# Kernel optimization log

Measured on AMD Instinct MI355X. Metric: run time of the kernel, lower is better.

The kernel has to match this reference:

```python
import jax, jax.numpy as jnp
import numpy as np

B, T, D, H = 16, 81, 128, 8  # batch, ntok, d_model (= d_head), n_head


def setup_inputs() -> dict:
    key = jax.random.key(0)
    ks = jax.random.split(key, 6)
    s = 0.02
    return {
        "x": jax.random.normal(ks[0], (B, T, D), jnp.float32),
        "msk": jnp.ones((1, H, T, T), jnp.float32),
        "wqkv_w": jax.random.normal(ks[1], (H * 2 * D, D), jnp.float32) * s,
        "wqkv_b": jax.random.normal(ks[2], (H * 2 * D,), jnp.float32) * s,
        "wk_w": jax.random.normal(ks[3], (H, D), jnp.float32) * s,
        "fanout_w": jax.random.normal(ks[4], (D, D), jnp.float32) * s,
        "fanout_b": jax.random.normal(ks[5], (D,), jnp.float32) * s,
        "head_enabled": jnp.ones((H,), jnp.float32),
        "n": 0, "layer": 0, "pas": 1,
    }


def quick_gelu(x):
    return x * jax.nn.sigmoid(1.702 * x)


def reference(x, msk, wqkv_w, wqkv_b, wk_w, fanout_w, fanout_b, head_enabled, n, layer, pas):
    b, t, d = x.shape
    h = wk_w.shape[0]
    # qkv projection: per-head q and v of full width d (d_head == d_model)
    y = x @ wqkv_w.T + wqkv_b                      # [b, t, h*2*d]
    y = y.reshape(b, t, h, 2 * d)
    q, v = y[..., :d], y[..., d:]                  # [b, t, h, d] each
    # k: input gated per-head by wk.weight rows
    k = x[:, :, None, :] * wk_w[None, None, :, :]  # [b, t, h, d]
    # v gating by head-enabled flags
    v = v * head_enabled[None, None, :, None]
    # L1 attention scores: a[b,h,t,s] = -sum_d |q[b,t,h,d] - k[b,s,h,d]| / sqrt(d)
    diff = jnp.abs(q[:, :, None, :, :] - k[:, None, :, :, :])  # [b, t, s, h, d]
    a = -diff.sum(-1)                               # [b, t, s, h]
    a = jnp.transpose(a, (0, 3, 1, 2)) / jnp.sqrt(jnp.asarray(d, x.dtype))  # [b,h,t,s]
    a = jax.nn.softmax(a, axis=3) * msk
    bo = jnp.einsum('bhts,bshd->bthd', a, v)        # [b, t, h, d]
    bo = bo.sum(axis=2)                             # sum over heads -> [b, t, d]
    ap = jnp.transpose(a[0] - 1.0 + msk[0], (1, 2, 0))  # [t, s, h]
    z = quick_gelu(bo + 4.0) - 4.0
    z = z @ fanout_w.T + fanout_b
    return (x + z, ap)
```

## Files before the change

### kernel.cpp

```cpp
#include <hip/hip_runtime.h>
#include <math.h>

#define Bq 16
#define Tq 81
#define Dq 128
#define Hq 8
#define BT (Bq*Tq)
#define BTD (Bq*Tq*Dq)
#define PS 84
#define P_SZ   (Bq*Tq*Hq*PS)
#define QV_SZ  (BT*Hq*Dq)
#define P_OFF  0
#define Q_OFF  (P_OFF + P_SZ)
#define V_OFF  (Q_OFF + QV_SZ)

#define LSTR 136

typedef __attribute__((ext_vector_type(8))) short short8;
typedef __attribute__((ext_vector_type(4))) float f32x4;
typedef _Float16 h2 __attribute__((ext_vector_type(2)));

__device__ __forceinline__ int imin(int a, int b) { return a < b ? a : b; }
__device__ __forceinline__ unsigned short f2bf(float f) {
    unsigned u = __float_as_uint(f);
    u += 0x7fffu + ((u >> 16) & 1u);
    return (unsigned short)(u >> 16);
}
__device__ __forceinline__ float bf2f(unsigned short s) {
    return __uint_as_float((unsigned)s << 16);
}
__device__ __forceinline__ unsigned pk2h(float a, float b) {
    h2 v; v[0] = (_Float16)a; v[1] = (_Float16)b;
    return *(unsigned*)&v;
}
__device__ __forceinline__ float l1h(unsigned qv, unsigned xv, unsigned wv, float acc) {
    const h2 q = *(const h2*)&qv, xx = *(const h2*)&xv, ww = *(const h2*)&wv;
    h2 d = q - xx * ww;
    unsigned du = (*(unsigned*)&d) & 0x7fff7fffu;
    const h2 da = *(const h2*)&du;
#if __has_builtin(__builtin_amdgcn_fdot2)
    return __builtin_amdgcn_fdot2(da, (h2){(_Float16)1.f, (_Float16)1.f}, acc, false);
#else
    return acc + (float)da[0] + (float)da[1];
#endif
}

__global__ __launch_bounds__(256) void k_qkv_mfma(
    const float* __restrict__ x, const float* __restrict__ wqkv,
    const float* __restrict__ bias, const float* __restrict__ he,
    float* __restrict__ Qo, unsigned short* __restrict__ Vb)
{
    __shared__ unsigned short xs[64 * LSTR];
    __shared__ unsigned short wsh[64 * LSTR];
    const int tid = threadIdx.x;
    const int w = tid >> 6, lane = tid & 63;
    const int ln = lane & 15, quad = lane >> 4;
    const int r0 = blockIdx.x * 64;
    const int n0 = blockIdx.y * 64;
    const int h  = blockIdx.y >> 2;
    const int isV = (blockIdx.y >> 1) & 1;
    const int c0 = (blockIdx.y & 1) * 64;

    #pragma unroll
    for (int i = 0; i < 8; ++i) {
        const int idx = tid + i * 256;
        const int r = idx >> 5, c4 = idx & 31;
        const int gr = imin(r0 + r, BT - 1);
        const float4 v = *(const float4*)(x + (size_t)gr * Dq + c4 * 4);
        ushort4 o;
        o.x = f2bf(v.x); o.y = f2bf(v.y); o.z = f2bf(v.z); o.w = f2bf(v.w);
        *(ushort4*)(&xs[r * LSTR + c4 * 4]) = o;

        const float4 vw = *(const float4*)(wqkv + (size_t)(n0 + r) * Dq + c4 * 4);
        ushort4 ow;
        ow.x = f2bf(vw.x); ow.y = f2bf(vw.y); ow.z = f2bf(vw.z); ow.w = f2bf(vw.w);
        *(ushort4*)(&wsh[r * LSTR + c4 * 4]) = ow;
    }
    __syncthreads();

    const unsigned short* xa = xs + (w * 16 + ln) * LSTR + quad * 8;
    const unsigned short* wb = wsh + ln * LSTR + quad * 8;

    f32x4 acc[4];
    #pragma unroll
    for (int i = 0; i < 4; ++i) acc[i] = (f32x4){0.f, 0.f, 0.f, 0.f};

    #pragma unroll
    for (int kb = 0; kb < Dq; kb += 32) {
        const short8 af = *(const short8*)(xa + kb);
        #pragma unroll
        for (int nt = 0; nt < 4; ++nt) {
            const short8 bf = *(const short8*)(wb + nt * 16 * LSTR + kb);
            acc[nt] = __builtin_amdgcn_mfma_f32_16x16x32_bf16(af, bf, acc[nt], 0, 0, 0);
        }
    }

    const float scale = isV ? he[h] : 1.0f;
    const int gm0 = r0 + w * 16 + quad * 4;
    #pragma unroll
    for (int nt = 0; nt < 4; ++nt) {
        const float bn = bias[n0 + nt * 16 + ln];
        #pragma unroll
        for (int r = 0; r < 4; ++r) {
            const int gm = gm0 + r;
            if (gm < BT) {
                const int bb = gm / 81, tt = gm - bb * 81;
                const size_t o =
                    (((size_t)bb * Hq + h) * Tq + tt) * Dq + c0 + nt * 16 + ln;
                const float val = (acc[nt][r] + bn) * scale;
                if (isV) Vb[o] = f2bf(val);
                else     Qo[o] = val;
            }
        }
    }
}

__global__ __launch_bounds__(512) void k_attn_out(
    const float* __restrict__ x, const float* __restrict__ Q,
    const float* __restrict__ wk, const float* __restrict__ msk,
    const unsigned short* __restrict__ Vb, const float* __restrict__ fw,
    const float* __restrict__ fb, float* __restrict__ out)
{
    __shared__ unsigned short xlh[Tq * Dq];
    __shared__ unsigned short Qlh[Hq * Dq];
    __shared__ unsigned short wklh[Hq * Dq];
    __shared__ float Pl[Hq][PS];
    float* const bo = (float*)xlh;
    float* const zs = (float*)xlh + 1024;

    const int tid = threadIdx.x;
    const int t0 = blockIdx.x, b = blockIdx.y;
    const int w = tid >> 6, lane = tid & 63;

    for (int idx = tid; idx < Tq * 16; idx += 512) {
        const int r = idx >> 4, g8 = idx & 15;
        const float* src = x + (size_t)(b * Tq + r) * Dq + g8 * 8;
        const float4 a = *(const float4*)(src);
        const float4 c = *(const float4*)(src + 4);
        uint4 o;
        o.x = pk2h(a.x, a.y); o.y = pk2h(a.z, a.w);
        o.z = pk2h(c.x, c.y); o.w = pk2h(c.z, c.w);
        *(uint4*)(&xlh[r * Dq + ((g8 ^ (r & 7)) << 3)]) = o;
    }
    if (tid < 128) {
        const int hh = tid >> 4, g8 = tid & 15;
        const float* src = Q + (((size_t)b * Hq + hh) * Tq + t0) * Dq + g8 * 8;
        const float4 a = *(const float4*)(src);
        const float4 c = *(const float4*)(src + 4);
        uint4 o;
        o.x = pk2h(a.x, a.y); o.y = pk2h(a.z, a.w);
        o.z = pk2h(c.x, c.y); o.w = pk2h(c.z, c.w);
        *(uint4*)(&Qlh[hh * Dq + g8 * 8]) = o;
    }
    if (tid >= 256 && tid < 384) {
        const int t2 = tid - 256;
        const int hh = t2 >> 4, g8 = t2 & 15;
        const float* src = wk + (size_t)hh * Dq + g8 * 8;
        const float4 a = *(const float4*)(src);
        const float4 c = *(const float4*)(src + 4);
        uint4 o;
        o.x = pk2h(a.x, a.y); o.y = pk2h(a.z, a.w);
        o.z = pk2h(c.x, c.y); o.w = pk2h(c.z, c.w);
        *(uint4*)(&wklh[hh * Dq + g8 * 8]) = o;
    }
    __syncthreads();

    const unsigned short* wrow = wklh + w * Dq;
    const unsigned short* qrow = Qlh + w * Dq;
    const int sx = (lane & 7) << 3;
    float acc0 = 0.f, acc1 = 0.f;
    {
        const unsigned short* xrow = xlh + (size_t)lane * Dq;
        #pragma unroll 4
        for (int g8 = 0; g8 < 16; ++g8) {
            const uint4 kk = *(const uint4*)(xrow + ((g8 << 3) ^ sx));
            const uint4 wv = *(const uint4*)(wrow + (g8 << 3));
            const uint4 qq = *(const uint4*)(qrow + (g8 << 3));
            acc0 = l1h(qq.x, kk.x, wv.x, acc0);
            acc0 = l1h(qq.y, kk.y, wv.y, acc0);
            acc0 = l1h(qq.z, kk.z, wv.z, acc0);
            acc0 = l1h(qq.w, kk.w, wv.w, acc0);
        }
    }
    if (lane < Tq - 64) {
        const unsigned short* xrow = xlh + (size_t)(64 + lane) * Dq;
        #pragma unroll 4
        for (int g8 = 0; g8 < 16; ++g8) {
            const uint4 kk = *(const uint4*)(xrow + ((g8 << 3) ^ sx));
            const uint4 wv = *(const uint4*)(wrow + (g8 << 3));
            const uint4 qq = *(const uint4*)(qrow + (g8 << 3));
            acc1 = l1h(qq.x, kk.x, wv.x, acc1);
            acc1 = l1h(qq.y, kk.y, wv.y, acc1);
            acc1 = l1h(qq.z, kk.z, wv.z, acc1);
            acc1 = l1h(qq.w, kk.w, wv.w, acc1);
        }
    }

    {
        const float ns = -0.08838834764831845f;
        const bool has1 = (lane < Tq - 64);
        const float v0 = acc0 * ns;
        const float v1 = has1 ? acc1 * ns : -1e30f;
        float m = fmaxf(v0, v1);
        #pragma unroll
        for (int off = 32; off > 0; off >>= 1)
            m = fmaxf(m, __shfl_xor(m, off));
        const float e0 = __expf(v0 - m);
        const float e1 = has1 ? __expf(v1 - m) : 0.f;
        float ssum = e0 + e1;
        #pragma unroll
        for (int off = 32; off > 0; off >>= 1)
            ssum += __shfl_xor(ssum, off);
        const float rinv = 1.0f / ssum;
        const float* mrow = msk + ((size_t)w * Tq + t0) * Tq;
        const float mv0 = mrow[lane];
        const float p0 = e0 * rinv * mv0;
        Pl[w][lane] = p0;
        if (b == 0)
            out[BTD + ((size_t)t0 * Tq + lane) * Hq + w] = p0 - 1.0f + mv0;
        if (has1) {
            const float mv1 = mrow[64 + lane];
            const float p1 = e1 * rinv * mv1;
            Pl[w][64 + lane] = p1;
            if (b == 0)
                out[BTD + ((size_t)t0 * Tq + 64 + lane) * Hq + w] = p1 - 1.0f + mv1;
        }
        if (lane < 3) Pl[w][81 + lane] = 0.f;
    }
    __syncthreads();

    {
        const int d0 = lane * 2;
        float2 acc = make_float2(0.f, 0.f);
        const unsigned short* vp = Vb + (((size_t)b * Hq + w) * Tq) * Dq + d0;
        for (int s4 = 0; s4 < 20; ++s4) {
            const float4 p = *(const float4*)(&Pl[w][s4 * 4]);
            #pragma unroll
            for (int ss = 0; ss < 4; ++ss) {
                const int s = s4 * 4 + ss;
                const ushort2 uv = *(const ushort2*)(vp + (size_t)s * Dq);
                const float pv = ((const float*)&p)[ss];
                acc.x = fmaf(pv, bf2f(uv.x), acc.x);
                acc.y = fmaf(pv, bf2f(uv.y), acc.y);
            }
        }
        {
            const ushort2 uv = *(const ushort2*)(vp + (size_t)80 * Dq);
            const float pv = Pl[w][80];
            acc.x = fmaf(pv, bf2f(uv.x), acc.x);
            acc.y = fmaf(pv, bf2f(uv.y), acc.y);
        }
        bo[w * Dq + d0]     = acc.x;
        bo[w * Dq + d0 + 1] = acc.y;
    }
    __syncthreads();

    if (tid < Dq) {
        float s = 0.f;
        #pragma unroll
        for (int ww = 0; ww < 8; ++ww) s += bo[ww * Dq + tid];
        const float tt2 = s + 4.0f;
        const float sg = 1.0f / (1.0f + __expf(-1.702f * tt2));
        zs[tid] = tt2 * sg - 4.0f;
    }
    __syncthreads();

    if (tid < Dq) {
        const int n = tid;
        const float* fwr = fw + (size_t)n * Dq;
        float a0 = 0.f;
        #pragma unroll 8
        for (int k4 = 0; k4 < 32; ++k4) {
            const float4 w4 = *(const float4*)(fwr + k4 * 4);
            const float4 z0 = *(const float4*)(&zs[k4 * 4]);
            a0 += z0.x * w4.x + z0.y * w4.y + z0.z * w4.z + z0.w * w4.w;
        }
        const size_t o = ((size_t)b * Tq + t0) * Dq + n;
        out[o] = x[o] + a0 + fb[n];
    }
}

extern "C" void kernel_launch(void* const* d_in, const int* in_sizes, int n_in,
                              void* d_out, int out_size, void* d_ws, size_t ws_size,
                              hipStream_t stream) {
    const float* x        = (const float*)d_in[0];
    const float* msk      = (const float*)d_in[1];
    const float* wqkv_w   = (const float*)d_in[2];
    const float* wqkv_b   = (const float*)d_in[3];
    const float* wk_w     = (const float*)d_in[4];
    const float* fanout_w = (const float*)d_in[5];
    const float* fanout_b = (const float*)d_in[6];
    const float* he       = (const float*)d_in[7];
    float* out = (float*)d_out;
    float* ws  = (float*)d_ws;

    float* Q  = ws + Q_OFF;
    unsigned short* Vb = (unsigned short*)(ws + V_OFF);

    k_qkv_mfma<<<dim3(21, 32), 256, 0, stream>>>(x, wqkv_w, wqkv_b, he, Q, Vb);
    k_attn_out<<<dim3(Tq, 16), 512, 0, stream>>>(x, Q, wk_w, msk, Vb,
                                                 fanout_w, fanout_b, out);
}
```

Measured before the change: 111.6 us.

## Precompute swizzled fp16 x once, drop a barrier, split fanout dot across threads

```diff
diff --git a/kernel.cpp b/kernel.cpp
--- a/kernel.cpp
+++ b/kernel.cpp
@@ -8,11 +8,9 @@
 #define BT (Bq*Tq)
 #define BTD (Bq*Tq*Dq)
 #define PS 84
-#define P_SZ   (Bq*Tq*Hq*PS)
-#define QV_SZ  (BT*Hq*Dq)
-#define P_OFF  0
-#define Q_OFF  (P_OFF + P_SZ)
-#define V_OFF  (Q_OFF + QV_SZ)
+#define QV_SZ   (BT*Hq*Dq)
+#define V_OFFF  (QV_SZ)
+#define XH_OFFF (QV_SZ + QV_SZ/2)
 
 #define LSTR 136
 
@@ -48,7 +46,8 @@
 __global__ __launch_bounds__(256) void k_qkv_mfma(
     const float* __restrict__ x, const float* __restrict__ wqkv,
     const float* __restrict__ bias, const float* __restrict__ he,
-    float* __restrict__ Qo, unsigned short* __restrict__ Vb)
+    float* __restrict__ Qo, unsigned short* __restrict__ Vb,
+    unsigned short* __restrict__ xh)
 {
     __shared__ unsigned short xs[64 * LSTR];
     __shared__ unsigned short wsh[64 * LSTR];
@@ -76,6 +75,26 @@
         ow.x = f2bf(vw.x); ow.y = f2bf(vw.y); ow.z = f2bf(vw.z); ow.w = f2bf(vw.w);
         *(ushort4*)(&wsh[r * LSTR + c4 * 4]) = ow;
     }
+
+    if (blockIdx.y == 0) {
+        #pragma unroll
+        for (int i = 0; i < 4; ++i) {
+            const int idx = tid + i * 256;
+            const int r = idx >> 4, g8 = idx & 15;
+            const int gm = r0 + r;
+            if (gm < BT) {
+                const int bb = gm / 81, tt = gm - bb * 81;
+                const float* src = x + (size_t)gm * Dq + g8 * 8;
+                const float4 a = *(const float4*)(src);
+                const float4 c = *(const float4*)(src + 4);
+                uint4 o;
+                o.x = pk2h(a.x, a.y); o.y = pk2h(a.z, a.w);
+                o.z = pk2h(c.x, c.y); o.w = pk2h(c.z, c.w);
+                *(uint4*)(&xh[((size_t)(bb * Tq + tt)) * Dq +
+                              ((g8 ^ (tt & 7)) << 3)]) = o;
+            }
+        }
+    }
     __syncthreads();
 
     const unsigned short* xa = xs + (w * 16 + ln) * LSTR + quad * 8;
@@ -118,29 +137,26 @@
 __global__ __launch_bounds__(512) void k_attn_out(
     const float* __restrict__ x, const float* __restrict__ Q,
     const float* __restrict__ wk, const float* __restrict__ msk,
-    const unsigned short* __restrict__ Vb, const float* __restrict__ fw,
-    const float* __restrict__ fb, float* __restrict__ out)
+    const unsigned short* __restrict__ Vb, const unsigned short* __restrict__ xh,
+    const float* __restrict__ fw, const float* __restrict__ fb,
+    float* __restrict__ out)
 {
     __shared__ unsigned short xlh[Tq * Dq];
     __shared__ unsigned short Qlh[Hq * Dq];
     __shared__ unsigned short wklh[Hq * Dq];
     __shared__ float Pl[Hq][PS];
-    float* const bo = (float*)xlh;
-    float* const zs = (float*)xlh + 1024;
+    __shared__ float bo[Hq * Dq];
+    __shared__ float zs[Dq];
 
     const int tid = threadIdx.x;
     const int t0 = blockIdx.x, b = blockIdx.y;
     const int w = tid >> 6, lane = tid & 63;
 
-    for (int idx = tid; idx < Tq * 16; idx += 512) {
-        const int r = idx >> 4, g8 = idx & 15;
-        const float* src = x + (size_t)(b * Tq + r) * Dq + g8 * 8;
-        const float4 a = *(const float4*)(src);
-        const float4 c = *(const float4*)(src + 4);
-        uint4 o;
-        o.x = pk2h(a.x, a.y); o.y = pk2h(a.z, a.w);
-        o.z = pk2h(c.x, c.y); o.w = pk2h(c.z, c.w);
-        *(uint4*)(&xlh[r * Dq + ((g8 ^ (r & 7)) << 3)]) = o;
+    {
+        const uint4* src = (const uint4*)(xh + (size_t)b * Tq * Dq);
+        uint4* dst = (uint4*)xlh;
+        for (int idx = tid; idx < Tq * 16; idx += 512)
+            dst[idx] = src[idx];
     }
     if (tid < 128) {
         const int hh = tid >> 4, g8 = tid & 15;
@@ -225,14 +241,13 @@
             if (b == 0)
                 out[BTD + ((size_t)t0 * Tq + 64 + lane) * Hq + w] = p1 - 1.0f + mv1;
         }
-        if (lane < 3) Pl[w][81 + lane] = 0.f;
-    }
-    __syncthreads();
+    }
 
     {
         const int d0 = lane * 2;
         float2 acc = make_float2(0.f, 0.f);
         const unsigned short* vp = Vb + (((size_t)b * Hq + w) * Tq) * Dq + d0;
+        #pragma unroll 4
         for (int s4 = 0; s4 < 20; ++s4) {
             const float4 p = *(const float4*)(&Pl[w][s4 * 4]);
             #pragma unroll
@@ -265,18 +280,22 @@
     }
     __syncthreads();
 
-    if (tid < Dq) {
-        const int n = tid;
-        const float* fwr = fw + (size_t)n * Dq;
+    {
+        const int n = tid >> 2, kq = tid & 3;
+        const float* fwr = fw + (size_t)n * Dq + kq * 32;
         float a0 = 0.f;
-        #pragma unroll 8
-        for (int k4 = 0; k4 < 32; ++k4) {
+        #pragma unroll
+        for (int k4 = 0; k4 < 8; ++k4) {
             const float4 w4 = *(const float4*)(fwr + k4 * 4);
-            const float4 z0 = *(const float4*)(&zs[k4 * 4]);
+            const float4 z0 = *(const float4*)(&zs[kq * 32 + k4 * 4]);
             a0 += z0.x * w4.x + z0.y * w4.y + z0.z * w4.z + z0.w * w4.w;
         }
-        const size_t o = ((size_t)b * Tq + t0) * Dq + n;
-        out[o] = x[o] + a0 + fb[n];
+        a0 += __shfl_xor(a0, 1);
+        a0 += __shfl_xor(a0, 2);
+        if (kq == 0) {
+            const size_t o = ((size_t)b * Tq + t0) * Dq + n;
+            out[o] = x[o] + a0 + fb[n];
+        }
     }
 }
 
@@ -294,10 +313,11 @@
     float* out = (float*)d_out;
     float* ws  = (float*)d_ws;
 
-    float* Q  = ws + Q_OFF;
-    unsigned short* Vb = (unsigned short*)(ws + V_OFF);
-
-    k_qkv_mfma<<<dim3(21, 32), 256, 0, stream>>>(x, wqkv_w, wqkv_b, he, Q, Vb);
-    k_attn_out<<<dim3(Tq, 16), 512, 0, stream>>>(x, Q, wk_w, msk, Vb,
+    float* Q  = ws;
+    unsigned short* Vb = (unsigned short*)(ws + V_OFFF);
+    unsigned short* xh = (unsigned short*)(ws + XH_OFFF);
+
+    k_qkv_mfma<<<dim3(21, 32), 256, 0, stream>>>(x, wqkv_w, wqkv_b, he, Q, Vb, xh);
+    k_attn_out<<<dim3(Tq, 16), 512, 0, stream>>>(x, Q, wk_w, msk, Vb, xh,
                                                  fanout_w, fanout_b, out);
 }
```

Measured after the change: 113.6 us. No clear change (+1.7%).
